# Optimization experiments

Measured on AMD Instinct MI355X. Metric: run time of the kernel, lower is better.

Reference implementation:

```python
import jax, jax.numpy as jnp
import numpy as np

BATCH, NUM, CONS = 16384, 512, 512


def setup_inputs() -> dict:
    key = jax.random.key(0)
    k1, k2, k3, k4 = jax.random.split(key, 4)
    preds = jax.random.uniform(k1, (BATCH, NUM), dtype=jnp.float32)
    # sparse, mutually-exclusive binary body masks (a literal is pos or neg, not both)
    r = jax.random.randint(k2, (CONS, NUM), 0, 12)
    pos_body = (r == 0).astype(jnp.float32)
    neg_body = (r == 1).astype(jnp.float32)
    head_atom = jax.random.randint(k3, (CONS,), 0, NUM).astype(jnp.int32)
    head_sign = jax.random.randint(k4, (CONS,), 0, 2).astype(jnp.bool_)
    return {"preds": preds, "pos_body": pos_body, "neg_body": neg_body,
            "head_atom": head_atom, "head_sign": head_sign}


def reference(preds, pos_body, neg_body, head_atom, head_sign):
    # apply_iterative with goal=None: Gauss-Seidel sweep over constraints.
    # For constraint c: body value per atom j is pos_body[c,j]*(1-p[:,j]) or
    # neg_body[c,j]*p[:,j]; candidate = 1 - max(0, max_j body value);
    # then head literal is raised (positive) or lowered (negative).
    def step(p, xs):
        pos_row, neg_row, atom, sign = xs
        # [batch, num] elementwise; masks are disjoint so per-atom max == concat-max
        vals = jnp.maximum(pos_row[None, :] * (1.0 - p), neg_row[None, :] * p)
        cand = 1.0 - jnp.maximum(jnp.max(vals, axis=1), 0.0)  # zeros column in torch cat
        prev = jnp.take(p, atom, axis=1)  # [batch]
        upd = jnp.where(sign,
                        jnp.maximum(prev, cand),
                        jnp.minimum(prev, 1.0 - cand))
        p = jax.lax.dynamic_update_slice(p, upd[:, None], (0, atom))
        return p, None

    out, _ = jax.lax.scan(step, preds, (pos_body, neg_body, head_atom, head_sign))
    return out
```

## Files before the change

kernel.cpp:

```cpp
#include <hip/hip_runtime.h>

#define BATCH 16384
#define NUM   512
#define CONS  512
#define ROWS  8
#define ZOFF  (NUM*16)
#define OOFF  (NUM*16 + 16)
#define LDSB  (NUM*16 + 32)
#define NPAD  (CONS + 4)
#define RSTR  84

typedef _Float16 h2 __attribute__((ext_vector_type(2)));
static __device__ __forceinline__ h2 u2h(unsigned u){ return __builtin_bit_cast(h2,u); }
static __device__ __forceinline__ unsigned h2u(h2 h){ return __builtin_bit_cast(unsigned,h); }
static __device__ __forceinline__ h2 hmax2(h2 a,h2 b){ return __builtin_elementwise_max(a,b); }
static __device__ __forceinline__ h2 hmin2(h2 a,h2 b){ return __builtin_elementwise_min(a,b); }
template<int C>
static __device__ __forceinline__ h2 rormax(h2 x) {
  unsigned v = (unsigned)__builtin_amdgcn_mov_dpp((int)h2u(x), C, 0xF, 0xF, true);
  return hmax2(x, u2h(v));
}

__global__ __launch_bounds__(64) void prep_kernel(
    const float* __restrict__ pos, const float* __restrict__ neg,
    const int* __restrict__ head_atom, const int* __restrict__ head_sign,
    unsigned* __restrict__ ents) {
  int c = blockIdx.x, lane = threadIdx.x;
  unsigned* rec = ents + (size_t)c * RSTR;
  if (c >= CONS) {
    for (int t = lane; t < RSTR; t += 64) {
      unsigned v = 0;
      if (t < 32) v = 0x20002000u;
      else if (t < 64) v = 0x20102010u;
      else if (t == 64) v = 0x8000u << 16;
      else if (t < 73) v = ZOFF;
      else if (t < 81) v = OOFF;
      rec[t] = v;
    }
    return;
  }
  __shared__ unsigned short LN[96], LP[96];
  __shared__ unsigned short slotN[64], slotP[64];
  __shared__ unsigned char usedN[64], usedP[64];
  __shared__ unsigned short spill[16][8];
  __shared__ int spn[16];
  __shared__ unsigned short exN[8], exP[8];
  __shared__ int exn, exp_;
  slotN[lane] = ZOFF; slotP[lane] = OOFF;
  usedN[lane] = 0;    usedP[lane] = 0;
  if (lane < 8) { exN[lane] = ZOFF; exP[lane] = OOFF; }
  if (lane < 16) spn[lane] = 0;
  __syncthreads();

  int hp1 = (c >= 1) ? head_atom[c-1] : -1;
  int hp2 = (c >= 2) ? head_atom[c-2] : -1;
  int nN = 0, nP = 0;
  bool fN1=false, fP1=false, fN2=false, fP2=false;
  for (int k = 0; k < NUM/64; ++k) {
    int a = k*64 + lane;
    bool ln = neg[(size_t)c*NUM + a] != 0.f;
    bool lp = pos[(size_t)c*NUM + a] != 0.f;
    bool n1 = ln && (a == hp1), n2 = ln && (a == hp2);
    bool p1 = lp && (a == hp1), p2 = lp && (a == hp2);
    fN1 |= (__ballot(n1) != 0ull); fN2 |= (__ballot(n2) != 0ull);
    fP1 |= (__ballot(p1) != 0ull); fP2 |= (__ballot(p2) != 0ull);
    bool kn = ln && !n1 && !n2;
    bool kp = lp && !p1 && !p2;
    unsigned long long mn = __ballot(kn), mp = __ballot(kp);
    unsigned long long lt = (1ull << lane) - 1ull;
    int rn = nN + (int)__popcll(mn & lt);
    int rp = nP + (int)__popcll(mp & lt);
    if (kn && rn < 96) LN[rn] = (unsigned short)a;
    if (kp && rp < 96) LP[rp] = (unsigned short)a;
    nN += (int)__popcll(mn);
    nP += (int)__popcll(mp);
  }
  __syncthreads();
  if (lane < 16) {
    int r = lane & 7;
    bool isP = lane >= 8;
    const unsigned short* L = isP ? LP : LN;
    int n = isP ? nP : nN; if (n > 96) n = 96;
    unsigned short* slot = isP ? slotP : slotN;
    unsigned char* used = isP ? usedP : usedN;
    int rr = 0;
    for (int t = 0; t < n; ++t) {
      int a = L[t];
      if ((a & 7) == r) {
        if (rr < 8) { int s = rr*8 + r; slot[s] = (unsigned short)(a*16); used[s] = 1; }
        else if (rr < 16) spill[lane][rr-8] = (unsigned short)(a*16);
        ++rr;
      }
    }
    spn[lane] = rr > 8 ? (rr > 16 ? 8 : rr - 8) : 0;
  }
  __syncthreads();
  if (lane < 2) {
    bool isP = lane == 1;
    unsigned short* slot = isP ? slotP : slotN;
    unsigned char* used = isP ? usedP : usedN;
    unsigned short* exb = isP ? exP : exN;
    int base = isP ? 8 : 0;
    int e = 0, scan = 0;
    for (int r = 0; r < 8; ++r) {
      int ns = spn[base + r];
      for (int k = 0; k < ns; ++k) {
        unsigned short v = spill[base + r][k];
        while (scan < 64 && used[scan]) ++scan;
        if (scan < 64) { slot[scan] = v; used[scan] = 1; }
        else if (e < 8) exb[e++] = v;
      }
    }
    if (isP) exp_ = e; else exn = e;
  }
  __syncthreads();

  int hc = head_atom[c];
  unsigned fl = 0;
  if (head_sign[c]) fl |= 1u;
  if (fN1) fl |= 2u;  if (fP1) fl |= 4u;
  if (fN2) fl |= 8u;  if (fP2) fl |= 16u;
  if (hc == hp1) fl |= 32u; else if (hc == hp2) fl |= 64u;
  fl |= ((unsigned)exn << 7) | ((unsigned)exp_ << 11);
  unsigned ho = (unsigned)hc * 16u;
  for (int t = lane; t < RSTR; t += 64) {
    unsigned v;
    if (t < 32) {
      int jp = t >> 4, g = t & 15;
      v = (unsigned)slotN[32*jp + g] | ((unsigned)slotN[32*jp + 16 + g] << 16);
    } else if (t < 64) {
      int tp = t - 32, jp = tp >> 4, g = tp & 15;
      v = (unsigned)slotP[32*jp + g] | ((unsigned)slotP[32*jp + 16 + g] << 16);
    } else if (t == 64) v = ho | (fl << 16);
    else if (t < 73) v = exN[t - 65];
    else if (t < 81) v = exP[t - 73];
    else v = 0;
    rec[t] = v;
  }
}

struct ENT { unsigned w0, w1, w2, w3, mh; };
struct RDv { h2 n0,n1,n2,n3,p0,p1,p2,p3,pv; unsigned mh; };
struct ST  { h2 braw, prevraw; unsigned ho, flu; };

static __device__ __forceinline__ ENT ldent(const unsigned* ents, int c, int g) {
  const unsigned* rec = ents + (size_t)c * RSTR;
  ENT e;
  e.w0 = rec[g]; e.w1 = rec[16+g]; e.w2 = rec[32+g]; e.w3 = rec[48+g];
  e.mh = rec[64];
  return e;
}
static __device__ __forceinline__ void issue_reads(const ENT& E, const char* Pb,
                                                   unsigned pr4, RDv& R) {
  R.n0 = *(const h2*)(Pb + ((E.w0 & 0xFFFFu) + pr4));
  R.n1 = *(const h2*)(Pb + ((E.w0 >> 16)     + pr4));
  R.n2 = *(const h2*)(Pb + ((E.w1 & 0xFFFFu) + pr4));
  R.n3 = *(const h2*)(Pb + ((E.w1 >> 16)     + pr4));
  R.p0 = *(const h2*)(Pb + ((E.w2 & 0xFFFFu) + pr4));
  R.p1 = *(const h2*)(Pb + ((E.w2 >> 16)     + pr4));
  R.p2 = *(const h2*)(Pb + ((E.w3 & 0xFFFFu) + pr4));
  R.p3 = *(const h2*)(Pb + ((E.w3 >> 16)     + pr4));
  R.pv = *(const h2*)(Pb + ((E.mh & 0xFFFFu) + pr4));
  R.mh = E.mh;
}
static __device__ __forceinline__ void combine(const RDv& R, const unsigned* ents,
                                               int c, const char* Pb, unsigned pr4, ST& S) {
  h2 aN = hmax2(hmax2(R.n0, R.n1), hmax2(R.n2, R.n3));
  h2 aP = hmin2(hmin2(R.p0, R.p1), hmin2(R.p2, R.p3));
  unsigned flu = ((unsigned)__builtin_amdgcn_readfirstlane((int)R.mh)) >> 16;
  if (flu & 0x7F80u) {
    const unsigned* rec = ents + (size_t)c * RSTR;
    unsigned xn = (flu >> 7) & 15u, xp = (flu >> 11) & 15u;
    for (unsigned j = 0; j < xn; ++j) aN = hmax2(aN, *(const h2*)(Pb + (rec[65+j] + pr4)));
    for (unsigned j = 0; j < xp; ++j) aP = hmin2(aP, *(const h2*)(Pb + (rec[73+j] + pr4)));
  }
  const h2 one2 = {(_Float16)1.f, (_Float16)1.f};
  h2 bp = hmax2(aN, one2 - aP);
  bp = rormax<0x121>(bp);
  bp = rormax<0x122>(bp);
  bp = rormax<0x124>(bp);
  bp = rormax<0x128>(bp);
  S.braw = bp; S.prevraw = R.pv; S.ho = R.mh & 0xFFFFu; S.flu = flu;
}
static __device__ __forceinline__ h2 finalize(const ST& S, h2 up1, h2 up2,
                                              char* Pb, unsigned pr4, int lane) {
  const h2 one2 = {(_Float16)1.f, (_Float16)1.f};
  unsigned fl = S.flu;
  unsigned mN1 = 0u-((fl>>1)&1u), mP1 = 0u-((fl>>2)&1u);
  unsigned mN2 = 0u-((fl>>3)&1u), mP2 = 0u-((fl>>4)&1u);
  h2 b = S.braw;
  b = hmax2(b, u2h(h2u(up1) & mN1));
  b = hmax2(b, u2h(h2u(one2 - up1) & mP1));
  b = hmax2(b, u2h(h2u(up2) & mN2));
  b = hmax2(b, u2h(h2u(one2 - up2) & mP2));
  unsigned mR1 = 0u-((fl>>5)&1u), mR2 = 0u-((fl>>6)&1u), mRn = ~(mR1|mR2);
  h2 prev = u2h((h2u(up1)&mR1) | (h2u(up2)&mR2) | (h2u(S.prevraw)&mRn));
  unsigned ms = 0u-(fl&1u);
  unsigned hi = h2u(hmax2(prev, one2 - b));
  unsigned lo = h2u(hmin2(prev, b));
  h2 upd = u2h((hi&ms) | (lo&~ms));
  if ((lane & 15) == 0 && !(fl & 0x8000u))
    *(h2*)(Pb + S.ho + pr4) = upd;
  return upd;
}

__global__ __launch_bounds__(64, 2) void solve_kernel(
    const float* __restrict__ preds,
    const unsigned* __restrict__ ents,
    float* __restrict__ out) {
  __shared__ char Pb[LDSB];
  const int lane = threadIdx.x;
  const unsigned pr4 = (unsigned)(lane >> 4) * 4u;
  const int r2 = lane >> 4, cs = lane & 15;
  const size_t row0 = (size_t)blockIdx.x * ROWS;

  if (lane < 4)      *(unsigned*)(Pb + ZOFF + lane*4) = 0u;
  else if (lane < 8) *(unsigned*)(Pb + OOFF + (lane-4)*4) = 0x3C003C00u;

  for (int i = 0; i < 16; ++i) {
    int a = i*32 + cs*2;
    float2 v0 = *(const float2*)(preds + (row0 + 2*r2)     * NUM + a);
    float2 v1 = *(const float2*)(preds + (row0 + 2*r2 + 1) * NUM + a);
    h2 w0 = {(_Float16)v0.x, (_Float16)v1.x};
    h2 w1 = {(_Float16)v0.y, (_Float16)v1.y};
    *(h2*)(Pb + a*16 + r2*4) = w0;
    *(h2*)(Pb + (a+1)*16 + r2*4) = w1;
  }
  __syncthreads();

  const int g = lane & 15;
  ENT E0 = ldent(ents, 0, g), E1 = ldent(ents, 1, g);
  ENT E2 = ldent(ents, 2, g), E3 = ldent(ents, 3, g);
  RDv RA, RB; ST S0, S1;
  issue_reads(E0, Pb, pr4, RA);
  issue_reads(E1, Pb, pr4, RB);
  combine(RA, ents, 0, Pb, pr4, S0);
  h2 up1 = (h2)0.0f, up2 = (h2)0.0f;

  #pragma unroll 1
  for (int i = 0; i < CONS; i += 2) {
    issue_reads(E2, Pb, pr4, RA);
    { h2 u = finalize(S0, up1, up2, Pb, pr4, lane); up2 = up1; up1 = u; }
    combine(RB, ents, i+1, Pb, pr4, S1);
    E2 = ldent(ents, i+4, g);
    issue_reads(E3, Pb, pr4, RB);
    { h2 u = finalize(S1, up1, up2, Pb, pr4, lane); up2 = up1; up1 = u; }
    combine(RA, ents, i+2, Pb, pr4, S0);
    E3 = ldent(ents, i+5, g);
  }

  __syncthreads();
  for (int i = 0; i < 16; ++i) {
    int a = i*32 + cs*2;
    h2 w0 = *(const h2*)(Pb + a*16 + r2*4);
    h2 w1 = *(const h2*)(Pb + (a+1)*16 + r2*4);
    float2 v0 = {(float)w0.x, (float)w1.x};
    float2 v1 = {(float)w0.y, (float)w1.y};
    *(float2*)(out + (row0 + 2*r2)     * NUM + a) = v0;
    *(float2*)(out + (row0 + 2*r2 + 1) * NUM + a) = v1;
  }
}

extern "C" void kernel_launch(void* const* d_in, const int* in_sizes, int n_in,
                              void* d_out, int out_size, void* d_ws, size_t ws_size,
                              hipStream_t stream) {
  (void)in_sizes; (void)n_in; (void)out_size; (void)ws_size;
  const float* preds     = (const float*)d_in[0];
  const float* pos       = (const float*)d_in[1];
  const float* neg       = (const float*)d_in[2];
  const int*   head_atom = (const int*)d_in[3];
  const int*   head_sign = (const int*)d_in[4];

  unsigned* ents = (unsigned*)d_ws;

  prep_kernel<<<NPAD, 64, 0, stream>>>(pos, neg, head_atom, head_sign, ents);
  solve_kernel<<<BATCH / ROWS, 64, 0, stream>>>(preds, ents, (float*)d_out);
}
```

Baseline: 280.3 us.

## Remap lane-to-slot layout to spread LDS banks and cheapen cross-lane reduction

Lanes are remapped so each row-pair group spans lanes 0-7 and 32-39, not 16 contiguous lanes. Padding slots for zero/one dummy reads are spread across 8 distinct 16-byte addresses, so dummy reads no longer hit the same LDS bank. The max-reduction now uses quad-permute and row-shift DPP plus permlane32_swap to match the new lane grouping. Finalize also skips the neighbour-dependency masking when the flags are clear, which risks divergence overhead and depends on the new lane mapping being consistent everywhere.

```diff
diff --git a/kernel.cpp b/kernel.cpp
--- a/kernel.cpp
+++ b/kernel.cpp
@@ -5,8 +5,8 @@
 #define CONS  512
 #define ROWS  8
 #define ZOFF  (NUM*16)
-#define OOFF  (NUM*16 + 16)
-#define LDSB  (NUM*16 + 32)
+#define OOFF  (NUM*16 + 128)
+#define LDSB  (NUM*16 + 256)
 #define NPAD  (CONS + 4)
 #define RSTR  84
 
@@ -16,7 +16,7 @@
 static __device__ __forceinline__ h2 hmax2(h2 a,h2 b){ return __builtin_elementwise_max(a,b); }
 static __device__ __forceinline__ h2 hmin2(h2 a,h2 b){ return __builtin_elementwise_min(a,b); }
 template<int C>
-static __device__ __forceinline__ h2 rormax(h2 x) {
+static __device__ __forceinline__ h2 dppmax(h2 x) {
   unsigned v = (unsigned)__builtin_amdgcn_mov_dpp((int)h2u(x), C, 0xF, 0xF, true);
   return hmax2(x, u2h(v));
 }
@@ -30,8 +30,8 @@
   if (c >= CONS) {
     for (int t = lane; t < RSTR; t += 64) {
       unsigned v = 0;
-      if (t < 32) v = 0x20002000u;
-      else if (t < 64) v = 0x20102010u;
+      if (t < 32)      { unsigned d = ZOFF + (unsigned)(t & 7) * 16u; v = d | (d << 16); }
+      else if (t < 64) { unsigned d = OOFF + (unsigned)(t & 7) * 16u; v = d | (d << 16); }
       else if (t == 64) v = 0x8000u << 16;
       else if (t < 73) v = ZOFF;
       else if (t < 81) v = OOFF;
@@ -46,7 +46,8 @@
   __shared__ int spn[16];
   __shared__ unsigned short exN[8], exP[8];
   __shared__ int exn, exp_;
-  slotN[lane] = ZOFF; slotP[lane] = OOFF;
+  slotN[lane] = (unsigned short)(ZOFF + (lane & 7) * 16);
+  slotP[lane] = (unsigned short)(OOFF + (lane & 7) * 16);
   usedN[lane] = 0;    usedP[lane] = 0;
   if (lane < 8) { exN[lane] = ZOFF; exP[lane] = OOFF; }
   if (lane < 16) spn[lane] = 0;
@@ -176,30 +177,38 @@
   }
   const h2 one2 = {(_Float16)1.f, (_Float16)1.f};
   h2 bp = hmax2(aN, one2 - aP);
-  bp = rormax<0x121>(bp);
-  bp = rormax<0x122>(bp);
-  bp = rormax<0x124>(bp);
-  bp = rormax<0x128>(bp);
+  bp = dppmax<0xB1>(bp);
+  bp = dppmax<0x4E>(bp);
+  bp = dppmax<0x141>(bp);
+  {
+    auto sw = __builtin_amdgcn_permlane32_swap((int)h2u(bp), (int)h2u(bp), false, false);
+    bp = hmax2(u2h((unsigned)sw[0]), u2h((unsigned)sw[1]));
+  }
   S.braw = bp; S.prevraw = R.pv; S.ho = R.mh & 0xFFFFu; S.flu = flu;
 }
 static __device__ __forceinline__ h2 finalize(const ST& S, h2 up1, h2 up2,
                                               char* Pb, unsigned pr4, int lane) {
   const h2 one2 = {(_Float16)1.f, (_Float16)1.f};
   unsigned fl = S.flu;
-  unsigned mN1 = 0u-((fl>>1)&1u), mP1 = 0u-((fl>>2)&1u);
-  unsigned mN2 = 0u-((fl>>3)&1u), mP2 = 0u-((fl>>4)&1u);
   h2 b = S.braw;
-  b = hmax2(b, u2h(h2u(up1) & mN1));
-  b = hmax2(b, u2h(h2u(one2 - up1) & mP1));
-  b = hmax2(b, u2h(h2u(up2) & mN2));
-  b = hmax2(b, u2h(h2u(one2 - up2) & mP2));
-  unsigned mR1 = 0u-((fl>>5)&1u), mR2 = 0u-((fl>>6)&1u), mRn = ~(mR1|mR2);
-  h2 prev = u2h((h2u(up1)&mR1) | (h2u(up2)&mR2) | (h2u(S.prevraw)&mRn));
+  if (fl & 0x1Eu) {
+    unsigned mN1 = 0u-((fl>>1)&1u), mP1 = 0u-((fl>>2)&1u);
+    unsigned mN2 = 0u-((fl>>3)&1u), mP2 = 0u-((fl>>4)&1u);
+    b = hmax2(b, u2h(h2u(up1) & mN1));
+    b = hmax2(b, u2h(h2u(one2 - up1) & mP1));
+    b = hmax2(b, u2h(h2u(up2) & mN2));
+    b = hmax2(b, u2h(h2u(one2 - up2) & mP2));
+  }
+  h2 prev = S.prevraw;
+  if (fl & 0x60u) {
+    unsigned mR1 = 0u-((fl>>5)&1u), mR2 = 0u-((fl>>6)&1u), mRn = ~(mR1|mR2);
+    prev = u2h((h2u(up1)&mR1) | (h2u(up2)&mR2) | (h2u(S.prevraw)&mRn));
+  }
   unsigned ms = 0u-(fl&1u);
   unsigned hi = h2u(hmax2(prev, one2 - b));
   unsigned lo = h2u(hmin2(prev, b));
   h2 upd = u2h((hi&ms) | (lo&~ms));
-  if ((lane & 15) == 0 && !(fl & 0x8000u))
+  if ((lane & 39) == 0 && !(fl & 0x8000u))
     *(h2*)(Pb + S.ho + pr4) = upd;
   return upd;
 }
@@ -210,25 +219,25 @@
     float* __restrict__ out) {
   __shared__ char Pb[LDSB];
   const int lane = threadIdx.x;
-  const unsigned pr4 = (unsigned)(lane >> 4) * 4u;
-  const int r2 = lane >> 4, cs = lane & 15;
+  const unsigned pr4 = (unsigned)((lane >> 3) & 3) * 4u;
+  const int g = (lane & 7) | ((lane >> 5) << 3);
+  const int r2s = lane >> 4, cs = lane & 15;
   const size_t row0 = (size_t)blockIdx.x * ROWS;
 
-  if (lane < 4)      *(unsigned*)(Pb + ZOFF + lane*4) = 0u;
-  else if (lane < 8) *(unsigned*)(Pb + OOFF + (lane-4)*4) = 0x3C003C00u;
+  if (lane < 32) *(unsigned*)(Pb + ZOFF + lane*4) = 0u;
+  else           *(unsigned*)(Pb + OOFF + (lane-32)*4) = 0x3C003C00u;
 
   for (int i = 0; i < 16; ++i) {
     int a = i*32 + cs*2;
-    float2 v0 = *(const float2*)(preds + (row0 + 2*r2)     * NUM + a);
-    float2 v1 = *(const float2*)(preds + (row0 + 2*r2 + 1) * NUM + a);
+    float2 v0 = *(const float2*)(preds + (row0 + 2*r2s)     * NUM + a);
+    float2 v1 = *(const float2*)(preds + (row0 + 2*r2s + 1) * NUM + a);
     h2 w0 = {(_Float16)v0.x, (_Float16)v1.x};
     h2 w1 = {(_Float16)v0.y, (_Float16)v1.y};
-    *(h2*)(Pb + a*16 + r2*4) = w0;
-    *(h2*)(Pb + (a+1)*16 + r2*4) = w1;
-  }
-  __syncthreads();
-
-  const int g = lane & 15;
+    *(h2*)(Pb + a*16 + r2s*4) = w0;
+    *(h2*)(Pb + (a+1)*16 + r2s*4) = w1;
+  }
+  __syncthreads();
+
   ENT E0 = ldent(ents, 0, g), E1 = ldent(ents, 1, g);
   ENT E2 = ldent(ents, 2, g), E3 = ldent(ents, 3, g);
   RDv RA, RB; ST S0, S1;
@@ -252,12 +261,12 @@
   __syncthreads();
   for (int i = 0; i < 16; ++i) {
     int a = i*32 + cs*2;
-    h2 w0 = *(const h2*)(Pb + a*16 + r2*4);
-    h2 w1 = *(const h2*)(Pb + (a+1)*16 + r2*4);
+    h2 w0 = *(const h2*)(Pb + a*16 + r2s*4);
+    h2 w1 = *(const h2*)(Pb + (a+1)*16 + r2s*4);
     float2 v0 = {(float)w0.x, (float)w1.x};
     float2 v1 = {(float)w0.y, (float)w1.y};
-    *(float2*)(out + (row0 + 2*r2)     * NUM + a) = v0;
-    *(float2*)(out + (row0 + 2*r2 + 1) * NUM + a) = v1;
+    *(float2*)(out + (row0 + 2*r2s)     * NUM + a) = v0;
+    *(float2*)(out + (row0 + 2*r2s + 1) * NUM + a) = v1;
   }
 }
 
```

After: 273.7 us. 1.02x faster.
